# Performance work log

Hardware: AMD Instinct MI355X
Metric: run time of the kernel (lower is better)

Reference implementation:

```python
import jax, jax.numpy as jnp
import numpy as np

B, IN_DIM, OUT_DIM = 262144, 2, 256


def setup_inputs() -> dict:
    key = jax.random.key(0)
    k1, k2, k3 = jax.random.split(key, 3)
    x = jax.random.normal(k1, (B, IN_DIM), dtype=jnp.float32)
    h = jax.random.normal(k2, (OUT_DIM, IN_DIM), dtype=jnp.float32) * 0.01
    delta = jax.random.normal(k3, (OUT_DIM,), dtype=jnp.float32) * 0.01
    return {"x": x, "h": h, "delta": delta}


def reference(x, h, delta):
    # z = F.linear(x, h): [B, OUT_DIM]
    theta = x @ h.T + delta  # phase argument, delta broadcast over batch
    out_real = jnp.cos(theta)
    out_imag = jnp.sin(theta)
    # S_proxy = diag_embed(mean_b out_complex); eigvals of a diagonal matrix
    # are its diagonal entries, so angles are arctan2(mean_imag, mean_real).
    mean_r = out_real.mean(axis=0)  # [OUT_DIM]
    mean_i = out_imag.mean(axis=0)  # [OUT_DIM]
    eta = jnp.sum(jnp.arctan2(mean_i, mean_r)) / jnp.pi
    return out_real, eta
```

## Files before the change

kernel.cpp:

```cpp
#include <hip/hip_runtime.h>
#include <math.h>


#define B_DIM 262144
#define O_DIM 256

typedef float vf4 __attribute__((ext_vector_type(4)));

__global__ __launch_bounds__(256) void fdc_main(
    const float* __restrict__ x, const float* __restrict__ h,
    const float* __restrict__ delta, float* __restrict__ out,
    float* __restrict__ partial ) {
  const int tid  = threadIdx.x;
  const int lane = tid & 63;
  const int rl   = tid >> 6;
  const int col4 = lane * 4;

  const float4* h4 = (const float4*)h;
  const float4 ha = h4[lane * 2];
  const float4 hb = h4[lane * 2 + 1];
  const float4 dl = ((const float4*)delta)[lane];

  const float2* x2 = (const float2*)x;
  vf4* out4 = (vf4*)out;

  float sc0 = 0.f, sc1 = 0.f, sc2 = 0.f, sc3 = 0.f;
  float ss0 = 0.f, ss1 = 0.f, ss2 = 0.f, ss3 = 0.f;

  const int stride = gridDim.x * 4;
  for (int row = blockIdx.x * 4 + rl; row < B_DIM; row += stride) {
    const float2 xv = x2[row];
    float s, c;
    vf4 o;
    const float t0 = fmaf(xv.x, ha.x, fmaf(xv.y, ha.y, dl.x));
    const float t1 = fmaf(xv.x, ha.z, fmaf(xv.y, ha.w, dl.y));
    const float t2 = fmaf(xv.x, hb.x, fmaf(xv.y, hb.y, dl.z));
    const float t3 = fmaf(xv.x, hb.z, fmaf(xv.y, hb.w, dl.w));
    __sincosf(t0, &s, &c); o.x = c; sc0 += c; ss0 += s;
    __sincosf(t1, &s, &c); o.y = c; sc1 += c; ss1 += s;
    __sincosf(t2, &s, &c); o.z = c; sc2 += c; ss2 += s;
    __sincosf(t3, &s, &c); o.w = c; sc3 += c; ss3 += s;
    __builtin_nontemporal_store(o, &out4[(size_t)row * 64 + lane]);
  }

  __shared__ float lds[4][512];
  lds[rl][col4 + 0] = sc0; lds[rl][col4 + 1] = sc1;
  lds[rl][col4 + 2] = sc2; lds[rl][col4 + 3] = sc3;
  lds[rl][256 + col4 + 0] = ss0; lds[rl][256 + col4 + 1] = ss1;
  lds[rl][256 + col4 + 2] = ss2; lds[rl][256 + col4 + 3] = ss3;
  __syncthreads();
  const float a = lds[0][tid] + lds[1][tid] + lds[2][tid] + lds[3][tid];
  const float b = lds[0][tid + 256] + lds[1][tid + 256] +
                  lds[2][tid + 256] + lds[3][tid + 256];
  float* p = partial + (size_t)blockIdx.x * 512;
  p[tid] = a;
  p[256 + tid] = b;
}

__global__ __launch_bounds__(256) void fdc_colred(
    const float* __restrict__ partial, int nb, float* __restrict__ angle) {
  const int o = blockIdx.x;
  const int t = threadIdx.x;
  float cs = 0.f, sn = 0.f;
  for (int b = t; b < nb; b += 256) {
    cs += partial[(size_t)b * 512 + o];
    sn += partial[(size_t)b * 512 + 256 + o];
  }
  __shared__ float rc[256], rs[256];
  rc[t] = cs; rs[t] = sn;
  __syncthreads();
  for (int st = 128; st > 0; st >>= 1) {
    if (t < st) { rc[t] += rc[t + st]; rs[t] += rs[t + st]; }
    __syncthreads();
  }
  if (t == 0) angle[o] = atan2f(rs[0], rc[0]);
}

__global__ __launch_bounds__(256) void fdc_final(
    const float* __restrict__ angle, float* __restrict__ out) {
  const int t = threadIdx.x;
  __shared__ float red[256];
  red[t] = angle[t];
  __syncthreads();
  for (int st = 128; st > 0; st >>= 1) {
    if (t < st) red[t] += red[t + st];
    __syncthreads();
  }
  if (t == 0) out[(size_t)B_DIM * O_DIM] = red[0] * (float)(1.0 / M_PI);
}

extern "C" void kernel_launch(void* const* d_in, const int* in_sizes, int n_in,
                              void* d_out, int out_size, void* d_ws, size_t ws_size,
                              hipStream_t stream) {
  const float* x     = (const float*)d_in[0];
  const float* h     = (const float*)d_in[1];
  const float* delta = (const float*)d_in[2];
  float* out = (float*)d_out;
  float* partial = (float*)d_ws;

  int nb = 2048;
  const size_t per_block = 512 * sizeof(float);
  while (nb > 1 && ws_size < (size_t)nb * per_block + 256 * sizeof(float))
    nb >>= 1;
  float* angle = partial + (size_t)nb * 512;

  fdc_main<<<nb, 256, 0, stream>>>(x, h, delta, out, partial);
  fdc_colred<<<256, 256, 0, stream>>>(partial, nb, angle);
  fdc_final<<<1, 256, 0, stream>>>(angle, out);
}
```

Measured before the change: 294.2 us.

## Halve main grid with 2-row unroll and restructure partial reduction into coalesced stages

The main kernel now launches a fixed 1024 blocks instead of up to 2048, and each wave handles two consecutive rows per iteration. This aims to add ILP and cut per-block overhead and the partial-sum traffic. The strided column reduction is replaced by a coalesced two-stage row reduction (64 blocks, then 1 block), with atan2 and the final sum fused into the last stage. This removes one launch and the uncoalesced reads. Workspace size is no longer checked, so a small workspace could overflow.

```diff
diff --git a/kernel.cpp b/kernel.cpp
--- a/kernel.cpp
+++ b/kernel.cpp
@@ -4,6 +4,8 @@
 
 #define B_DIM 262144
 #define O_DIM 256
+#define NB1 1024
+#define NB2 64
 
 typedef float vf4 __attribute__((ext_vector_type(4)));
 
@@ -27,20 +29,24 @@
   float sc0 = 0.f, sc1 = 0.f, sc2 = 0.f, sc3 = 0.f;
   float ss0 = 0.f, ss1 = 0.f, ss2 = 0.f, ss3 = 0.f;
 
-  const int stride = gridDim.x * 4;
-  for (int row = blockIdx.x * 4 + rl; row < B_DIM; row += stride) {
-    const float2 xv = x2[row];
-    float s, c;
-    vf4 o;
-    const float t0 = fmaf(xv.x, ha.x, fmaf(xv.y, ha.y, dl.x));
-    const float t1 = fmaf(xv.x, ha.z, fmaf(xv.y, ha.w, dl.y));
-    const float t2 = fmaf(xv.x, hb.x, fmaf(xv.y, hb.y, dl.z));
-    const float t3 = fmaf(xv.x, hb.z, fmaf(xv.y, hb.w, dl.w));
-    __sincosf(t0, &s, &c); o.x = c; sc0 += c; ss0 += s;
-    __sincosf(t1, &s, &c); o.y = c; sc1 += c; ss1 += s;
-    __sincosf(t2, &s, &c); o.z = c; sc2 += c; ss2 += s;
-    __sincosf(t3, &s, &c); o.w = c; sc3 += c; ss3 += s;
-    __builtin_nontemporal_store(o, &out4[(size_t)row * 64 + lane]);
+  const int stride = NB1 * 8;
+  for (int base = blockIdx.x * 8 + rl * 2; base < B_DIM; base += stride) {
+#pragma unroll
+    for (int k = 0; k < 2; ++k) {
+      const int row = base + k;
+      const float2 xv = x2[row];
+      float s, c;
+      vf4 o;
+      const float t0 = fmaf(xv.x, ha.x, fmaf(xv.y, ha.y, dl.x));
+      const float t1 = fmaf(xv.x, ha.z, fmaf(xv.y, ha.w, dl.y));
+      const float t2 = fmaf(xv.x, hb.x, fmaf(xv.y, hb.y, dl.z));
+      const float t3 = fmaf(xv.x, hb.z, fmaf(xv.y, hb.w, dl.w));
+      __sincosf(t0, &s, &c); o.x = c; sc0 += c; ss0 += s;
+      __sincosf(t1, &s, &c); o.y = c; sc1 += c; ss1 += s;
+      __sincosf(t2, &s, &c); o.z = c; sc2 += c; ss2 += s;
+      __sincosf(t3, &s, &c); o.w = c; sc3 += c; ss3 += s;
+      __builtin_nontemporal_store(o, &out4[(size_t)row * 64 + lane]);
+    }
   }
 
   __shared__ float lds[4][512];
@@ -57,30 +63,32 @@
   p[256 + tid] = b;
 }
 
-__global__ __launch_bounds__(256) void fdc_colred(
-    const float* __restrict__ partial, int nb, float* __restrict__ angle) {
-  const int o = blockIdx.x;
+__global__ __launch_bounds__(256) void fdc_red1(
+    const float* __restrict__ partial, float* __restrict__ partial2) {
+  const int t = threadIdx.x;
+  const float* base = partial + (size_t)blockIdx.x * (NB1 / NB2) * 512;
+  float cs = 0.f, sn = 0.f;
+#pragma unroll
+  for (int r = 0; r < NB1 / NB2; ++r) {
+    cs += base[r * 512 + t];
+    sn += base[r * 512 + 256 + t];
+  }
+  partial2[(size_t)blockIdx.x * 512 + t] = cs;
+  partial2[(size_t)blockIdx.x * 512 + 256 + t] = sn;
+}
+
+__global__ __launch_bounds__(256) void fdc_red2(
+    const float* __restrict__ partial2, float* __restrict__ out) {
   const int t = threadIdx.x;
   float cs = 0.f, sn = 0.f;
-  for (int b = t; b < nb; b += 256) {
-    cs += partial[(size_t)b * 512 + o];
-    sn += partial[(size_t)b * 512 + 256 + o];
+#pragma unroll 4
+  for (int r = 0; r < NB2; ++r) {
+    cs += partial2[(size_t)r * 512 + t];
+    sn += partial2[(size_t)r * 512 + 256 + t];
   }
-  __shared__ float rc[256], rs[256];
-  rc[t] = cs; rs[t] = sn;
-  __syncthreads();
-  for (int st = 128; st > 0; st >>= 1) {
-    if (t < st) { rc[t] += rc[t + st]; rs[t] += rs[t + st]; }
-    __syncthreads();
-  }
-  if (t == 0) angle[o] = atan2f(rs[0], rc[0]);
-}
-
-__global__ __launch_bounds__(256) void fdc_final(
-    const float* __restrict__ angle, float* __restrict__ out) {
-  const int t = threadIdx.x;
+  float ang = atan2f(sn, cs);
   __shared__ float red[256];
-  red[t] = angle[t];
+  red[t] = ang;
   __syncthreads();
   for (int st = 128; st > 0; st >>= 1) {
     if (t < st) red[t] += red[t + st];
@@ -96,15 +104,11 @@
   const float* h     = (const float*)d_in[1];
   const float* delta = (const float*)d_in[2];
   float* out = (float*)d_out;
-  float* partial = (float*)d_ws;
+  float* partial  = (float*)d_ws;
+  float* partial2 = partial + (size_t)NB1 * 512;
+  (void)ws_size;
 
-  int nb = 2048;
-  const size_t per_block = 512 * sizeof(float);
-  while (nb > 1 && ws_size < (size_t)nb * per_block + 256 * sizeof(float))
-    nb >>= 1;
-  float* angle = partial + (size_t)nb * 512;
-
-  fdc_main<<<nb, 256, 0, stream>>>(x, h, delta, out, partial);
-  fdc_colred<<<256, 256, 0, stream>>>(partial, nb, angle);
-  fdc_final<<<1, 256, 0, stream>>>(angle, out);
+  fdc_main<<<NB1, 256, 0, stream>>>(x, h, delta, out, partial);
+  fdc_red1<<<NB2, 256, 0, stream>>>(partial, partial2);
+  fdc_red2<<<1, 256, 0, stream>>>(partial2, out);
 }
```

Result: faster. 287.5 us (-2.3%).
